# Performance work log

Hardware: AMD Instinct MI355X
Metric: run time of the kernel (lower is better)

## Reference

```python
import jax, jax.numpy as jnp
import numpy as np

B, N, C, H, DFF = 4, 1024, 768, 12, 3072
D = C // H
EPS = 1e-5


def _layernorm(x, w, b, axes):
    mu = jnp.mean(x, axis=axes, keepdims=True)
    var = jnp.mean(jnp.square(x - mu), axis=axes, keepdims=True)
    return (x - mu) * jax.lax.rsqrt(var + EPS) * w + b


def setup_inputs() -> dict:
    key = jax.random.key(0)
    ks = jax.random.split(key, 8)
    s = lambda fan_in: 1.0 / np.sqrt(fan_in)
    return {
        'x': jax.random.normal(ks[0], (B, N, C), jnp.float32),
        'ln0_w': jnp.ones((C,), jnp.float32),
        'ln0_b': jnp.zeros((C,), jnp.float32),
        'qkv_w': jax.random.normal(ks[1], (3 * C, C), jnp.float32) * s(C),
        'qkv_b': jax.random.normal(ks[2], (3 * C,), jnp.float32) * 0.01,
        'proj_w': jax.random.normal(ks[3], (C, C), jnp.float32) * s(C),
        'proj_b': jax.random.normal(ks[4], (C,), jnp.float32) * 0.01,
        'attn_norm_w': jnp.ones((H, N, N), jnp.float32),
        'attn_norm_b': jnp.zeros((H, N, N), jnp.float32),
        'ln1_w': jnp.ones((C,), jnp.float32),
        'ln1_b': jnp.zeros((C,), jnp.float32),
        'fc1_w': jax.random.normal(ks[5], (DFF, C), jnp.float32) * s(C),
        'fc1_b': jax.random.normal(ks[6], (DFF,), jnp.float32) * 0.01,
        'fc2_w': jax.random.normal(ks[7], (C, DFF), jnp.float32) * s(DFF),
        'fc2_b': jnp.zeros((C,), jnp.float32),
    }


def reference(x, ln0_w, ln0_b, qkv_w, qkv_b, proj_w, proj_b,
              attn_norm_w, attn_norm_b, ln1_w, ln1_b,
              fc1_w, fc1_b, fc2_w, fc2_b):
    # pre-norm
    h = _layernorm(x, ln0_w, ln0_b, axes=-1)
    # qkv projection -> (3, B, H, N, D)
    qkv = (h @ qkv_w.T + qkv_b).reshape(B, N, 3, H, D).transpose(2, 0, 3, 1, 4)
    q, k, v = qkv[0], qkv[1], qkv[2]
    # grassmanian_point: project each head vector onto the unit sphere
    q = q / jnp.linalg.norm(q, axis=-1, keepdims=True)
    k = k / jnp.linalg.norm(k, axis=-1, keepdims=True)
    # sum_d (q_{id} k_{jd})^2  ==  (q^2) @ (k^2)^T   -- avoids (B,H,D,N,N) tensor
    attn = jnp.einsum('bhid,bhjd->bhij', jnp.square(q), jnp.square(k))
    # LayerNorm over (H, N, N) jointly per batch element
    attn = _layernorm(attn, attn_norm_w, attn_norm_b, axes=(1, 2, 3))
    out = jnp.einsum('bhij,bhjd->bhid', attn, v)
    out = out.transpose(0, 2, 1, 3).reshape(B, N, C)
    out = out @ proj_w.T + proj_b
    # residual + post-norm + FFN (dropout/drop_path are identity in eval)
    src = x + out
    src = _layernorm(src, ln1_w, ln1_b, axes=-1)
    ff = jax.nn.gelu(src @ fc1_w.T + fc1_b, approximate=False) @ fc2_w.T + fc2_b
    src = src + ff
    return src, attn
```

## Files before the change

### kernel.cpp

```cpp
#include <hip/hip_runtime.h>

typedef __bf16 bf16;
typedef __bf16 bf16x4 __attribute__((ext_vector_type(4)));
typedef __bf16 bf16x8 __attribute__((ext_vector_type(8)));
typedef float f32x4 __attribute__((ext_vector_type(4)));

#define DEVI __device__ __forceinline__

typedef const __attribute__((address_space(1))) void* gas1;
typedef __attribute__((address_space(3))) void* las3;

DEVI int xcd_chunk(int bid, int nwg)
{
  const int q = nwg >> 3, r = nwg & 7;
  const int xcd = bid & 7, rank = bid >> 3;
  return (xcd < r) ? xcd * (q + 1) + rank
                   : r * (q + 1) + (xcd - r) * q + rank;
}

DEVI void stage_tile(const bf16* g, int ld, char* lds, int bytes, int tid)
{
  const int wv = tid >> 6, lane = tid & 63;
  const char* gb = (const char*)g;
  const long rowb = (long)ld * 2;
  for (int off = wv * 1024; off < bytes; off += 4096) {
    const int o  = off + lane * 16;
    const int s  = o ^ (((o >> 7) & 7) << 4);
    const int r  = s >> 7;
    const int cb = s & 127;
    __builtin_amdgcn_global_load_lds((gas1)(gb + (long)r * rowb + cb),
                                     (las3)(lds + off), 16, 0, 0);
  }
}

template<int N> DEVI void waitvm()
{
  if constexpr (N == 8)      asm volatile("s_waitcnt vmcnt(8)" ::: "memory");
  else if constexpr (N == 6) asm volatile("s_waitcnt vmcnt(6)" ::: "memory");
  else if constexpr (N == 4) asm volatile("s_waitcnt vmcnt(4)" ::: "memory");
  else if constexpr (N == 2) asm volatile("s_waitcnt vmcnt(2)" ::: "memory");
  else                       asm volatile("s_waitcnt vmcnt(0)" ::: "memory");
}

DEVI void wave_lds_fence()
{
  asm volatile("s_waitcnt lgkmcnt(0)" ::: "memory");
  __builtin_amdgcn_sched_barrier(0);
}

struct EpiProj {
  const float* bias; const float* x; float* src;
  DEVI void operator()(int z, int row, int col, float v) const {
    const long i = (long)row * 768 + col;
    src[i] = v + bias[col] + x[i];
  }
};

struct EpiGelu {
  const float* bias; bf16* g;
  DEVI void operator()(int z, int row, int col, float v) const {
    const float t = v + bias[col];
    const float r = 0.5f * t * (1.0f + erff(t * 0.70710678118654752f));
    g[(long)row * 3072 + col] = (bf16)r;
  }
};

struct EpiOut {
  const float* bias; const float* lnf; float* outp;
  DEVI void operator()(int z, int row, int col, float v) const {
    const long i = (long)row * 768 + col;
    outp[i] = v + bias[col] + lnf[i];
  }
};

template<int BM, int BN, int WC, int FM, int FN, int WPE, class Epi>
__global__ __launch_bounds__(256, WPE) void gemm_k(
    const bf16* __restrict__ A, long abatch,
    const bf16* __restrict__ B, long bbatch,
    int lda, int ldb, int K, Epi epi)
{
  constexpr int BK = 64;
  constexpr int AB = BM * BK * 2, BB = BN * BK * 2;
  constexpr int BUFB = AB + BB;
  constexpr int LPS = BUFB / 4096;
  __shared__ char smem[2 * BUFB];

  const int tid = threadIdx.x, lane = tid & 63, wv = tid >> 6;
  const int wr = wv / WC, wc = wv % WC;
  const int NT = gridDim.x;
  const int nwg = NT * gridDim.y;
  const int wid = xcd_chunk(blockIdx.y * NT + blockIdx.x, nwg);
  const int mt = wid / NT, nt = wid % NT;
  const int z = blockIdx.z;
  const long abase = (long)z * abatch + (long)mt * BM * lda;
  const long bbase = (long)z * bbatch + (long)nt * BN * ldb;
  const int l15 = lane & 15;
  const int sw = (lane & 7) << 4;

  auto stage_all = [&](int buf, int kt) {
    char* base = smem + buf * BUFB;
    stage_tile(A + abase + kt, lda, base, AB, tid);
    stage_tile(B + bbase + kt, ldb, base + AB, BB, tid);
  };

  f32x4 acc[FM][FN];
#pragma unroll
  for (int m = 0; m < FM; ++m)
#pragma unroll
    for (int n = 0; n < FN; ++n) acc[m][n] = f32x4{0.f, 0.f, 0.f, 0.f};

  const int arow = wr * FM * 16, bcol = wc * FN * 16;
  const int T = K / BK;

  stage_all(0, 0);
  int cur = 0;
  for (int t = 0; t < T; ++t) {
    if (t + 1 < T) { stage_all(cur ^ 1, (t + 1) * BK); waitvm<LPS>(); }
    else           { waitvm<0>(); }
    __builtin_amdgcn_s_barrier();
    asm volatile("" ::: "memory");

    const char* As = smem + cur * BUFB;
    const char* Bs = As + AB;
#pragma unroll
    for (int ks = 0; ks < 2; ++ks) {
      const int ko = (ks * 64 + (lane >> 4) * 16) ^ sw;
      bf16x8 av[FM], bv[FN];
#pragma unroll
      for (int m = 0; m < FM; ++m)
        av[m] = *(const bf16x8*)(As + (arow + m * 16 + l15) * 128 + ko);
#pragma unroll
      for (int n = 0; n < FN; ++n)
        bv[n] = *(const bf16x8*)(Bs + (bcol + n * 16 + l15) * 128 + ko);
#pragma unroll
      for (int m = 0; m < FM; ++m)
#pragma unroll
        for (int n = 0; n < FN; ++n)
          acc[m][n] = __builtin_amdgcn_mfma_f32_16x16x32_bf16(av[m], bv[n], acc[m][n], 0, 0, 0);
    }
    asm volatile("s_waitcnt lgkmcnt(0)" ::: "memory");
    __builtin_amdgcn_s_barrier();
    asm volatile("" ::: "memory");
    cur ^= 1;
  }

#pragma unroll
  for (int m = 0; m < FM; ++m)
#pragma unroll
    for (int n = 0; n < FN; ++n)
#pragma unroll
      for (int r = 0; r < 4; ++r) {
        const int grow = mt * BM + arow + m * 16 + (lane >> 4) * 4 + r;
        const int gcol = nt * BN + bcol + n * 16 + l15;
        epi(z, grow, gcol, acc[m][n][r]);
      }
}

__global__ __launch_bounds__(256, 3) void gemm_qkv(
    const bf16* __restrict__ A, const bf16* __restrict__ B,
    const float* __restrict__ bias, bf16* __restrict__ q2h,
    bf16* __restrict__ k2h, bf16* __restrict__ vth)
{
  constexpr int BM = 128, BN = 64, BK = 64;
  constexpr int AB = BM * BK * 2, BB = BN * BK * 2;
  constexpr int BUFB = AB + BB;
  constexpr int LPS = BUFB / 4096;
  __shared__ char smem[2 * BUFB];
  __shared__ float rowsum[2][BM];

  const int tid = threadIdx.x, lane = tid & 63, wv = tid >> 6;
  const int wr = wv >> 1, wc = wv & 1;
  const int NT = 36;
  const int wid = xcd_chunk(blockIdx.y * NT + blockIdx.x, NT * 32);
  const int mt = wid / NT, nt = wid % NT;
  const int sec = nt / 12, h = nt - sec * 12;
  const long abase = (long)mt * BM * 768;
  const long bbase = (long)nt * BN * 768;
  const int l15 = lane & 15, lhi = lane >> 4;
  const int sw = (lane & 7) << 4;

  auto stage_all = [&](int buf, int kt) {
    char* base = smem + buf * BUFB;
    stage_tile(A + abase + kt, 768, base, AB, tid);
    stage_tile(B + bbase + kt, 768, base + AB, BB, tid);
  };

  f32x4 acc[4][2];
#pragma unroll
  for (int m = 0; m < 4; ++m)
#pragma unroll
    for (int n = 0; n < 2; ++n) acc[m][n] = f32x4{0.f, 0.f, 0.f, 0.f};

  const int arow = wr * 64, bcol = wc * 32;

  stage_all(0, 0);
  int cur = 0;
  for (int t = 0; t < 12; ++t) {
    if (t + 1 < 12) { stage_all(cur ^ 1, (t + 1) * BK); waitvm<LPS>(); }
    else            { waitvm<0>(); }
    __builtin_amdgcn_s_barrier();
    asm volatile("" ::: "memory");

    const char* As = smem + cur * BUFB;
    const char* Bs = As + AB;
#pragma unroll
    for (int ks = 0; ks < 2; ++ks) {
      const int ko = (ks * 64 + lhi * 16) ^ sw;
      bf16x8 av[4], bv[2];
#pragma unroll
      for (int m = 0; m < 4; ++m)
        av[m] = *(const bf16x8*)(As + (arow + m * 16 + l15) * 128 + ko);
#pragma unroll
      for (int n = 0; n < 2; ++n)
        bv[n] = *(const bf16x8*)(Bs + (bcol + n * 16 + l15) * 128 + ko);
#pragma unroll
      for (int m = 0; m < 4; ++m)
#pragma unroll
        for (int n = 0; n < 2; ++n)
          acc[m][n] = __builtin_amdgcn_mfma_f32_16x16x32_bf16(av[m], bv[n], acc[m][n], 0, 0, 0);
    }
    asm volatile("s_waitcnt lgkmcnt(0)" ::: "memory");
    __builtin_amdgcn_s_barrier();
    asm volatile("" ::: "memory");
    cur ^= 1;
  }

  float val[4][2][4];
#pragma unroll
  for (int m = 0; m < 4; ++m)
#pragma unroll
    for (int n = 0; n < 2; ++n)
#pragma unroll
      for (int r = 0; r < 4; ++r)
        val[m][n][r] = acc[m][n][r] + bias[nt * 64 + bcol + n * 16 + l15];

  if (sec < 2) {
#pragma unroll
    for (int m = 0; m < 4; ++m)
#pragma unroll
      for (int r = 0; r < 4; ++r) {
        float p = val[m][0][r] * val[m][0][r] + val[m][1][r] * val[m][1][r];
        p += __shfl_xor(p, 1);
        p += __shfl_xor(p, 2);
        p += __shfl_xor(p, 4);
        p += __shfl_xor(p, 8);
        if (l15 == 0) rowsum[wc][arow + m * 16 + lhi * 4 + r] = p;
      }
    __syncthreads();
    bf16* dst = (sec == 0) ? q2h : k2h;
#pragma unroll
    for (int m = 0; m < 4; ++m)
#pragma unroll
      for (int r = 0; r < 4; ++r) {
        const int row = arow + m * 16 + lhi * 4 + r;
        const float inv = 1.0f / (rowsum[0][row] + rowsum[1][row]);
        const int grow = mt * BM + row;
        const int b = grow >> 10, nn = grow & 1023;
        const long base = (((long)(b * 12 + h)) * 1024 + nn) * 64;
#pragma unroll
        for (int n = 0; n < 2; ++n) {
          const float v = val[m][n][r];
          dst[base + bcol + n * 16 + l15] = (bf16)(v * v * inv);
        }
      }
  } else {
    bf16* T = (bf16*)smem;
#pragma unroll
    for (int m = 0; m < 4; ++m)
#pragma unroll
      for (int n = 0; n < 2; ++n)
#pragma unroll
        for (int r = 0; r < 4; ++r) {
          const int row = arow + m * 16 + lhi * 4 + r;
          const int col = bcol + n * 16 + l15;
          T[col * 144 + row] = (bf16)val[m][n][r];
        }
    __syncthreads();
    const int bq = mt >> 3, nn0 = (mt & 7) * 128;
    const long basez = ((long)(bq * 12 + h) * 64) * 1024;
#pragma unroll
    for (int it = 0; it < 4; ++it) {
      const int flat = it * 2048 + tid * 8;
      const int d = flat >> 7, c = flat & 127;
      const bf16x8 o = *(const bf16x8*)&T[d * 144 + c];
      *(bf16x8*)&vth[basez + (long)d * 1024 + nn0 + c] = o;
    }
  }
}

__global__ __launch_bounds__(256, 3) void attn_fused(
    const bf16* __restrict__ q2h, const bf16* __restrict__ k2h,
    const bf16* __restrict__ vth, const float* __restrict__ stats,
    const float* __restrict__ wn, const float* __restrict__ bn,
    float* __restrict__ attn_out, bf16* __restrict__ oh)
{
  __shared__ char smem[49152];
  char* Qs  = smem;
  char* Ks0 = smem + 8192;
  char* Ks1 = smem + 16384;
  char* Vs0 = smem + 24576;
  char* Vs1 = smem + 32768;
  char* Pall = smem + 40960;

  const int tid = threadIdx.x, lane = tid & 63, wv = tid >> 6;
  const int wid = xcd_chunk(blockIdx.x, 768);
  const int b = wid & 3;
  const int mt = (wid >> 2) & 15;
  const int h = wid >> 6;
  const int zq = b * 12 + h;
  const float mu = stats[2 * b], rs = stats[2 * b + 1];
  const int l15 = lane & 15, lhi = lane >> 4;
  const int sw = (lane & 7) << 4;
  char* Ps = Pall + wv * 2048;

  const long zoff = (long)zq * 65536;

  auto load_wb = [&](int nt, f32x4* wreg, f32x4* breg) {
#pragma unroll
    for (int rr = 0; rr < 4; ++rr) {
      const long grow = (long)mt * 64 + wv * 16 + rr * 4 + lhi;
      const long gcol = (long)nt * 64 + l15 * 4;
      wreg[rr] = *(const f32x4*)&wn[((long)h * 1024 + grow) * 1024 + gcol];
      breg[rr] = *(const f32x4*)&bn[((long)h * 1024 + grow) * 1024 + gcol];
    }
  };

  f32x4 wcur[4], bcur[4];
  load_wb(0, wcur, bcur);
  stage_tile(q2h + zoff + (long)mt * 4096, 64, Qs, 8192, tid);
  stage_tile(k2h + zoff, 64, Ks0, 8192, tid);
  stage_tile(vth + zoff, 1024, Vs0, 8192, tid);
  __syncthreads();

  f32x4 oacc[4];
#pragma unroll
  for (int n = 0; n < 4; ++n) oacc[n] = f32x4{0.f, 0.f, 0.f, 0.f};

  for (int nt = 0; nt < 16; ++nt) {
    const int cur = nt & 1;
    char* Kc = cur ? Ks1 : Ks0;
    char* Vc = cur ? Vs1 : Vs0;
    char* Kn = cur ? Ks0 : Ks1;
    char* Vn = cur ? Vs0 : Vs1;

    f32x4 wnx[4], bnx[4];
    if (nt + 1 < 16) {
      load_wb(nt + 1, wnx, bnx);
      stage_tile(k2h + zoff + (long)(nt + 1) * 4096, 64, Kn, 8192, tid);
      stage_tile(vth + zoff + (nt + 1) * 64, 1024, Vn, 8192, tid);
    }

    f32x4 acc[4];
#pragma unroll
    for (int n = 0; n < 4; ++n) acc[n] = f32x4{0.f, 0.f, 0.f, 0.f};
    __builtin_amdgcn_s_setprio(1);
#pragma unroll
    for (int ks = 0; ks < 2; ++ks) {
      const int ko = (ks * 64 + lhi * 16) ^ sw;
      const bf16x8 av = *(const bf16x8*)(Qs + (wv * 16 + l15) * 128 + ko);
#pragma unroll
      for (int n = 0; n < 4; ++n) {
        const bf16x8 bv = *(const bf16x8*)(Kc + (n * 16 + l15) * 128 + ko);
        acc[n] = __builtin_amdgcn_mfma_f32_16x16x32_bf16(av, bv, acc[n], 0, 0, 0);
      }
    }
    __builtin_amdgcn_s_setprio(0);
#pragma unroll
    for (int n = 0; n < 4; ++n)
#pragma unroll
      for (int r = 0; r < 4; ++r) {
        const int row = lhi * 4 + r;
        const int cb = (n * 32 + l15 * 2) ^ ((row & 7) << 4);
        *(bf16*)(Ps + row * 128 + cb) = (bf16)((acc[n][r] - mu) * rs);
      }
    wave_lds_fence();

#pragma unroll
    for (int rr = 0; rr < 4; ++rr) {
      const int row = rr * 4 + lhi;
      const int cb = (l15 * 8) ^ ((row & 7) << 4);
      const bf16x4 s4 = *(const bf16x4*)(Ps + row * 128 + cb);
      const long grow = (long)mt * 64 + wv * 16 + row;
      const long gcol = (long)nt * 64 + l15 * 4;
      f32x4 r4;
      bf16x4 h4;
#pragma unroll
      for (int e = 0; e < 4; ++e) {
        const float r = (float)s4[e] * wcur[rr][e] + bcur[rr][e];
        r4[e] = r;
        h4[e] = (bf16)r;
      }
      *(f32x4*)&attn_out[((long)zq * 1024 + grow) * 1024 + gcol] = r4;
      *(bf16x4*)(Ps + row * 128 + cb) = h4;
    }
    wave_lds_fence();

    __builtin_amdgcn_s_setprio(1);
#pragma unroll
    for (int ks = 0; ks < 2; ++ks) {
      const int ko = (ks * 64 + lhi * 16) ^ sw;
      const bf16x8 av = *(const bf16x8*)(Ps + l15 * 128 + ko);
#pragma unroll
      for (int n = 0; n < 4; ++n) {
        const bf16x8 bv = *(const bf16x8*)(Vc + (n * 16 + l15) * 128 + ko);
        oacc[n] = __builtin_amdgcn_mfma_f32_16x16x32_bf16(av, bv, oacc[n], 0, 0, 0);
      }
    }
    __builtin_amdgcn_s_setprio(0);
    waitvm<4>();
    __builtin_amdgcn_s_barrier();
    asm volatile("" ::: "memory");

    if (nt + 1 < 16) {
#pragma unroll
      for (int rr = 0; rr < 4; ++rr) { wcur[rr] = wnx[rr]; bcur[rr] = bnx[rr]; }
    }
  }

#pragma unroll
  for (int n = 0; n < 4; ++n)
#pragma unroll
    for (int r = 0; r < 4; ++r) {
      const int row = mt * 64 + wv * 16 + lhi * 4 + r;
      const int col = n * 16 + l15;
      oh[((long)(b * 1024 + row)) * 768 + h * 64 + col] = (bf16)oacc[n][r];
    }
}

__global__ void cast_all(const float* __restrict__ qkvw, const float* __restrict__ projw,
                         const float* __restrict__ fc1w, const float* __restrict__ fc2w,
                         bf16* __restrict__ dq, bf16* __restrict__ dp,
                         bf16* __restrict__ d1, bf16* __restrict__ d2)
{
  const int i = blockIdx.x * 256 + threadIdx.x;
  const float* s; bf16* d; int off;
  if (i < 442368)       { s = qkvw; d = dq; off = i; }
  else if (i < 589824)  { s = projw; d = dp; off = i - 442368; }
  else if (i < 1179648) { s = fc1w; d = d1; off = i - 589824; }
  else                  { s = fc2w; d = d2; off = i - 1179648; }
  const f32x4 v = *(const f32x4*)&s[(long)off * 4];
  bf16x4 o;
#pragma unroll
  for (int j = 0; j < 4; ++j) o[j] = (bf16)v[j];
  *(bf16x4*)&d[(long)off * 4] = o;
}

__global__ __launch_bounds__(256) void ln_row(
    const float* __restrict__ in, const float* __restrict__ w,
    const float* __restrict__ b, bf16* __restrict__ outh,
    float* __restrict__ outf)
{
  __shared__ float red[256];
  const int row = blockIdx.x, tid = threadIdx.x;
  const float* p = in + (long)row * 768;
  const float v0 = p[tid], v1 = p[tid + 256], v2 = p[tid + 512];
  red[tid] = v0 + v1 + v2;
  __syncthreads();
  for (int st = 128; st > 0; st >>= 1) { if (tid < st) red[tid] += red[tid + st]; __syncthreads(); }
  const float mu = red[0] * (1.0f / 768.0f);
  __syncthreads();
  const float d0 = v0 - mu, d1 = v1 - mu, d2 = v2 - mu;
  red[tid] = d0 * d0 + d1 * d1 + d2 * d2;
  __syncthreads();
  for (int st = 128; st > 0; st >>= 1) { if (tid < st) red[tid] += red[tid + st]; __syncthreads(); }
  const float rs = rsqrtf(red[0] * (1.0f / 768.0f) + 1e-5f);
  const float dv[3] = {d0, d1, d2};
#pragma unroll
  for (int k = 0; k < 3; ++k) {
    const int c = tid + k * 256;
    const float h = dv[k] * rs * w[c] + b[c];
    outh[(long)row * 768 + c] = (bf16)h;
    if (outf) outf[(long)row * 768 + c] = h;
  }
}

__global__ __launch_bounds__(256) void stats_accum(
    const bf16* __restrict__ q2h, const bf16* __restrict__ k2h,
    float* __restrict__ Gq, float* __restrict__ Gk,
    float* __restrict__ Sq, float* __restrict__ Sk)
{
  __shared__ float rowbuf[8][128];
  const int tid = threadIdx.x;
  const int z = blockIdx.y;
  const long base = ((long)z * 1024 + (long)blockIdx.x * 128) * 64;
  const int tx = tid & 15, ty = tid >> 4;
  float gq[4][4] = {}, gk[4][4] = {};
  float sq = 0.f, sk = 0.f;
  for (int r0 = 0; r0 < 128; r0 += 8) {
    __syncthreads();
    {
      const int idx = tid * 4;
      const int rr = idx >> 7, cc = idx & 127;
      const long a = base + (long)(r0 + rr) * 64 + (cc & 63);
      const bf16x4 v4 = (cc < 64) ? *(const bf16x4*)&q2h[a]
                                  : *(const bf16x4*)&k2h[a];
#pragma unroll
      for (int j = 0; j < 4; ++j) rowbuf[rr][cc + j] = (float)v4[j];
    }
    __syncthreads();
#pragma unroll
    for (int r = 0; r < 8; ++r) {
      float qa[4], qe[4], ka[4], ke[4];
#pragma unroll
      for (int i = 0; i < 4; ++i) {
        qa[i] = rowbuf[r][ty * 4 + i]; qe[i] = rowbuf[r][tx * 4 + i];
        ka[i] = rowbuf[r][64 + ty * 4 + i]; ke[i] = rowbuf[r][64 + tx * 4 + i];
      }
#pragma unroll
      for (int i = 0; i < 4; ++i)
#pragma unroll
        for (int j = 0; j < 4; ++j) {
          gq[i][j] += qa[i] * qe[j];
          gk[i][j] += ka[i] * ke[j];
        }
    }
    if (tid < 128) {
      float s = 0.f;
#pragma unroll
      for (int r = 0; r < 8; ++r) s += rowbuf[r][tid];
      if (tid < 64) sq += s; else sk += s;
    }
  }
#pragma unroll
  for (int i = 0; i < 4; ++i)
#pragma unroll
    for (int j = 0; j < 4; ++j) {
      atomicAdd(&Gq[(long)z * 4096 + (ty * 4 + i) * 64 + tx * 4 + j], gq[i][j]);
      atomicAdd(&Gk[(long)z * 4096 + (ty * 4 + i) * 64 + tx * 4 + j], gk[i][j]);
    }
  if (tid < 64) atomicAdd(&Sq[z * 64 + tid], sq);
  else if (tid < 128) atomicAdd(&Sk[z * 64 + tid - 64], sk);
}

__global__ __launch_bounds__(256) void stats_final(
    const float* __restrict__ Gq, const float* __restrict__ Gk,
    const float* __restrict__ Sq, const float* __restrict__ Sk,
    float* __restrict__ stats)
{
  __shared__ double red[256];
  const int b = blockIdx.x, tid = threadIdx.x;
  double s2 = 0.0, s1 = 0.0;
  for (int h = 0; h < 12; ++h) {
    const float* gq = Gq + ((long)(b * 12 + h)) * 4096;
    const float* gk = Gk + ((long)(b * 12 + h)) * 4096;
    for (int i = tid; i < 4096; i += 256) s2 += (double)gq[i] * (double)gk[i];
    const float* sqp = Sq + (b * 12 + h) * 64;
    const float* skp = Sk + (b * 12 + h) * 64;
    for (int i = tid; i < 64; i += 256) s1 += (double)sqp[i] * (double)skp[i];
  }
  red[tid] = s2; __syncthreads();
  for (int st = 128; st > 0; st >>= 1) { if (tid < st) red[tid] += red[tid + st]; __syncthreads(); }
  const double S2 = red[0]; __syncthreads();
  red[tid] = s1; __syncthreads();
  for (int st = 128; st > 0; st >>= 1) { if (tid < st) red[tid] += red[tid + st]; __syncthreads(); }
  if (tid == 0) {
    const double S1 = red[0];
    const double cnt = 12.0 * 1024.0 * 1024.0;
    const double mean = S1 / cnt;
    const double var = S2 / cnt - mean * mean;
    stats[2 * b] = (float)mean;
    stats[2 * b + 1] = (float)(1.0 / sqrt(var + 1e-5));
  }
}

extern "C" void kernel_launch(void* const* d_in, const int* in_sizes, int n_in,
                              void* d_out, int out_size, void* d_ws, size_t ws_size,
                              hipStream_t stream)
{
  const float* x      = (const float*)d_in[0];
  const float* ln0_w  = (const float*)d_in[1];
  const float* ln0_b  = (const float*)d_in[2];
  const float* qkv_w  = (const float*)d_in[3];
  const float* qkv_b  = (const float*)d_in[4];
  const float* proj_w = (const float*)d_in[5];
  const float* proj_b = (const float*)d_in[6];
  const float* attn_w = (const float*)d_in[7];
  const float* attn_b = (const float*)d_in[8];
  const float* ln1_w  = (const float*)d_in[9];
  const float* ln1_b  = (const float*)d_in[10];
  const float* fc1_w  = (const float*)d_in[11];
  const float* fc1_b  = (const float*)d_in[12];
  const float* fc2_w  = (const float*)d_in[13];
  const float* fc2_b  = (const float*)d_in[14];

  float* out_src  = (float*)d_out;
  float* out_attn = out_src + 4L * 1024 * 768;

  char* p = (char*)d_ws;
  auto take = [&](long bytes) -> char* {
    char* r = p;
    p += (bytes + 255) & ~255L;
    return r;
  };
  bf16* qkvw_h = (bf16*)take(3538944);
  bf16* projw_h = (bf16*)take(1179648);
  bf16* fc1w_h = (bf16*)take(4718592);
  bf16* fc2w_h = (bf16*)take(4718592);
  char* regB = take(12582912);
  bf16* hh = (bf16*)regB;
  float* src = (float*)regB;
  char* regC = take(37748736);
  bf16* gact = (bf16*)regC;
  float* ln1f = (float*)(regC + 25165824);
  bf16* q2h = (bf16*)take(6291456);
  bf16* k2h = (bf16*)take(6291456);
  bf16* vth = (bf16*)take(6291456);
  bf16* oh  = (bf16*)take(6291456);
  bf16* h1v = (bf16*)take(6291456);
  float* Gq = (float*)take(786432);
  float* Gk = (float*)take(786432);
  float* Sq = (float*)take(12288);
  float* Sk = (float*)take(12288);
  float* stats = (float*)take(256);

  const dim3 blk(256);

  (void)hipMemsetAsync((void*)Gq, 0, 786432 * 2 + 12288 * 2 + 256, stream);

  cast_all<<<dim3(1769472 / 256), blk, 0, stream>>>(
      qkv_w, proj_w, fc1_w, fc2_w, qkvw_h, projw_h, fc1w_h, fc2w_h);

  ln_row<<<dim3(4096), blk, 0, stream>>>(x, ln0_w, ln0_b, hh, nullptr);

  gemm_qkv<<<dim3(36, 32), blk, 0, stream>>>(
      hh, qkvw_h, qkv_b, q2h, k2h, vth);

  stats_accum<<<dim3(8, 48), blk, 0, stream>>>(q2h, k2h, Gq, Gk, Sq, Sk);
  stats_final<<<dim3(4), blk, 0, stream>>>(Gq, Gk, Sq, Sk, stats);

  attn_fused<<<dim3(768), blk, 0, stream>>>(
      q2h, k2h, vth, stats, attn_w, attn_b, out_attn, oh);

  gemm_k<128, 64, 2, 4, 2, 3, EpiProj><<<dim3(12, 32, 1), blk, 0, stream>>>(
      oh, 0, projw_h, 0, 768, 768, 768, EpiProj{proj_b, x, src});

  ln_row<<<dim3(4096), blk, 0, stream>>>(src, ln1_w, ln1_b, h1v, ln1f);

  gemm_k<128, 64, 2, 4, 2, 3, EpiGelu><<<dim3(48, 32, 1), blk, 0, stream>>>(
      h1v, 0, fc1w_h, 0, 768, 768, 768, EpiGelu{fc1_b, gact});

  gemm_k<128, 64, 2, 4, 2, 3, EpiOut><<<dim3(12, 32, 1), blk, 0, stream>>>(
      gact, 0, fc2w_h, 0, 3072, 3072, 3072, EpiOut{fc2_b, ln1f, out_src});
}
```

Baseline: 364.9 us.

## Fuse Gram statistics into QKV GEMM epilogue and merge weight cast with LayerNorm

The q²/k² Gram matrices and column sums used for the attention LayerNorm statistics are now computed inside the QKV GEMM epilogue. Each tile is staged into swizzled LDS, multiplied with MFMA and accumulated with atomics, which removes the separate stats_accum kernel and its re-read of q2h/k2h. The weight cast and the first LayerNorm are also merged into one prep launch to cut a kernel launch. In exchange the GEMM epilogue does extra LDS traffic, MFMA work and many more global atomics per tile.

```diff
diff --git a/kernel.cpp b/kernel.cpp
--- a/kernel.cpp
+++ b/kernel.cpp
@@ -159,7 +159,9 @@
 __global__ __launch_bounds__(256, 3) void gemm_qkv(
     const bf16* __restrict__ A, const bf16* __restrict__ B,
     const float* __restrict__ bias, bf16* __restrict__ q2h,
-    bf16* __restrict__ k2h, bf16* __restrict__ vth)
+    bf16* __restrict__ k2h, bf16* __restrict__ vth,
+    float* __restrict__ Gq, float* __restrict__ Gk,
+    float* __restrict__ Sq, float* __restrict__ Sk)
 {
   constexpr int BM = 128, BN = 64, BK = 64;
   constexpr int AB = BM * BK * 2, BB = BN * BK * 2;
@@ -247,7 +249,15 @@
         if (l15 == 0) rowsum[wc][arow + m * 16 + lhi * 4 + r] = p;
       }
     __syncthreads();
+
     bf16* dst = (sec == 0) ? q2h : k2h;
+    float* G  = (sec == 0) ? Gq  : Gk;
+    float* S  = (sec == 0) ? Sq  : Sk;
+    const int bq = mt >> 3;
+    const int z = bq * 12 + h;
+    char* T0 = smem;
+    char* T1 = smem + 8192;
+    float colsum[2] = {0.f, 0.f};
 #pragma unroll
     for (int m = 0; m < 4; ++m)
 #pragma unroll
@@ -255,14 +265,47 @@
         const int row = arow + m * 16 + lhi * 4 + r;
         const float inv = 1.0f / (rowsum[0][row] + rowsum[1][row]);
         const int grow = mt * BM + row;
-        const int b = grow >> 10, nn = grow & 1023;
-        const long base = (((long)(b * 12 + h)) * 1024 + nn) * 64;
+        const int nn = grow & 1023;
+        const long base = (((long)z) * 1024 + nn) * 64;
+        char* Tt = (row & 64) ? T1 : T0;
+        const int np = row & 63;
 #pragma unroll
         for (int n = 0; n < 2; ++n) {
           const float v = val[m][n][r];
-          dst[base + bcol + n * 16 + l15] = (bf16)(v * v * inv);
+          const int d = bcol + n * 16 + l15;
+          const bf16 q2b = (bf16)(v * v * inv);
+          dst[base + d] = q2b;
+          *(bf16*)(Tt + d * 128 + ((np * 2) ^ ((d & 7) << 4))) = q2b;
+          colsum[n] += (float)q2b;
         }
       }
+#pragma unroll
+    for (int n = 0; n < 2; ++n) {
+      float s = colsum[n];
+      s += __shfl_xor(s, 16);
+      s += __shfl_xor(s, 32);
+      if (lane < 16) atomicAdd(&S[z * 64 + bcol + n * 16 + l15], s);
+    }
+    __syncthreads();
+
+#pragma unroll
+    for (int gi = 0; gi < 4; ++gi) {
+      const int g = wv * 4 + gi;
+      const int dr = g >> 2, ec = g & 3;
+      f32x4 ga = f32x4{0.f, 0.f, 0.f, 0.f};
+#pragma unroll
+      for (int ks = 0; ks < 4; ++ks) {
+        const char* Tt = (ks & 2) ? T1 : T0;
+        const int ko = ((ks & 1) * 64 + lhi * 16) ^ sw;
+        const bf16x8 av = *(const bf16x8*)(Tt + (dr * 16 + l15) * 128 + ko);
+        const bf16x8 bv = *(const bf16x8*)(Tt + (ec * 16 + l15) * 128 + ko);
+        ga = __builtin_amdgcn_mfma_f32_16x16x32_bf16(av, bv, ga, 0, 0, 0);
+      }
+#pragma unroll
+      for (int r = 0; r < 4; ++r)
+        atomicAdd(&G[(long)z * 4096 + (dr * 16 + lhi * 4 + r) * 64 + ec * 16 + l15],
+                  ga[r]);
+    }
   } else {
     bf16* T = (bf16*)smem;
 #pragma unroll
@@ -427,22 +470,49 @@
     }
 }
 
-__global__ void cast_all(const float* __restrict__ qkvw, const float* __restrict__ projw,
-                         const float* __restrict__ fc1w, const float* __restrict__ fc2w,
-                         bf16* __restrict__ dq, bf16* __restrict__ dp,
-                         bf16* __restrict__ d1, bf16* __restrict__ d2)
-{
-  const int i = blockIdx.x * 256 + threadIdx.x;
-  const float* s; bf16* d; int off;
-  if (i < 442368)       { s = qkvw; d = dq; off = i; }
-  else if (i < 589824)  { s = projw; d = dp; off = i - 442368; }
-  else if (i < 1179648) { s = fc1w; d = d1; off = i - 589824; }
-  else                  { s = fc2w; d = d2; off = i - 1179648; }
-  const f32x4 v = *(const f32x4*)&s[(long)off * 4];
-  bf16x4 o;
-#pragma unroll
-  for (int j = 0; j < 4; ++j) o[j] = (bf16)v[j];
-  *(bf16x4*)&d[(long)off * 4] = o;
+__global__ __launch_bounds__(256) void prep(
+    const float* __restrict__ qkvw, const float* __restrict__ projw,
+    const float* __restrict__ fc1w, const float* __restrict__ fc2w,
+    bf16* __restrict__ dq, bf16* __restrict__ dp,
+    bf16* __restrict__ d1, bf16* __restrict__ d2,
+    const float* __restrict__ x, const float* __restrict__ w,
+    const float* __restrict__ bb, bf16* __restrict__ outh)
+{
+  __shared__ float red[256];
+  const int bid = blockIdx.x, tid = threadIdx.x;
+  if (bid < 6912) {
+    const int i = bid * 256 + tid;
+    const float* s; bf16* d; int off;
+    if (i < 442368)       { s = qkvw; d = dq; off = i; }
+    else if (i < 589824)  { s = projw; d = dp; off = i - 442368; }
+    else if (i < 1179648) { s = fc1w; d = d1; off = i - 589824; }
+    else                  { s = fc2w; d = d2; off = i - 1179648; }
+    const f32x4 v = *(const f32x4*)&s[(long)off * 4];
+    bf16x4 o;
+#pragma unroll
+    for (int j = 0; j < 4; ++j) o[j] = (bf16)v[j];
+    *(bf16x4*)&d[(long)off * 4] = o;
+  } else {
+    const int row = bid - 6912;
+    const float* p = x + (long)row * 768;
+    const float v0 = p[tid], v1 = p[tid + 256], v2 = p[tid + 512];
+    red[tid] = v0 + v1 + v2;
+    __syncthreads();
+    for (int st = 128; st > 0; st >>= 1) { if (tid < st) red[tid] += red[tid + st]; __syncthreads(); }
+    const float mu = red[0] * (1.0f / 768.0f);
+    __syncthreads();
+    const float d0 = v0 - mu, d1v = v1 - mu, d2v = v2 - mu;
+    red[tid] = d0 * d0 + d1v * d1v + d2v * d2v;
+    __syncthreads();
+    for (int st = 128; st > 0; st >>= 1) { if (tid < st) red[tid] += red[tid + st]; __syncthreads(); }
+    const float rs = rsqrtf(red[0] * (1.0f / 768.0f) + 1e-5f);
+    const float dv[3] = {d0, d1v, d2v};
+#pragma unroll
+    for (int k = 0; k < 3; ++k) {
+      const int c = tid + k * 256;
+      outh[(long)row * 768 + c] = (bf16)(dv[k] * rs * w[c] + bb[c]);
+    }
+  }
 }
 
 __global__ __launch_bounds__(256) void ln_row(
@@ -472,64 +542,6 @@
     outh[(long)row * 768 + c] = (bf16)h;
     if (outf) outf[(long)row * 768 + c] = h;
   }
-}
-
-__global__ __launch_bounds__(256) void stats_accum(
-    const bf16* __restrict__ q2h, const bf16* __restrict__ k2h,
-    float* __restrict__ Gq, float* __restrict__ Gk,
-    float* __restrict__ Sq, float* __restrict__ Sk)
-{
-  __shared__ float rowbuf[8][128];
-  const int tid = threadIdx.x;
-  const int z = blockIdx.y;
-  const long base = ((long)z * 1024 + (long)blockIdx.x * 128) * 64;
-  const int tx = tid & 15, ty = tid >> 4;
-  float gq[4][4] = {}, gk[4][4] = {};
-  float sq = 0.f, sk = 0.f;
-  for (int r0 = 0; r0 < 128; r0 += 8) {
-    __syncthreads();
-    {
-      const int idx = tid * 4;
-      const int rr = idx >> 7, cc = idx & 127;
-      const long a = base + (long)(r0 + rr) * 64 + (cc & 63);
-      const bf16x4 v4 = (cc < 64) ? *(const bf16x4*)&q2h[a]
-                                  : *(const bf16x4*)&k2h[a];
-#pragma unroll
-      for (int j = 0; j < 4; ++j) rowbuf[rr][cc + j] = (float)v4[j];
-    }
-    __syncthreads();
-#pragma unroll
-    for (int r = 0; r < 8; ++r) {
-      float qa[4], qe[4], ka[4], ke[4];
-#pragma unroll
-      for (int i = 0; i < 4; ++i) {
-        qa[i] = rowbuf[r][ty * 4 + i]; qe[i] = rowbuf[r][tx * 4 + i];
-        ka[i] = rowbuf[r][64 + ty * 4 + i]; ke[i] = rowbuf[r][64 + tx * 4 + i];
-      }
-#pragma unroll
-      for (int i = 0; i < 4; ++i)
-#pragma unroll
-        for (int j = 0; j < 4; ++j) {
-          gq[i][j] += qa[i] * qe[j];
-          gk[i][j] += ka[i] * ke[j];
-        }
-    }
-    if (tid < 128) {
-      float s = 0.f;
-#pragma unroll
-      for (int r = 0; r < 8; ++r) s += rowbuf[r][tid];
-      if (tid < 64) sq += s; else sk += s;
-    }
-  }
-#pragma unroll
-  for (int i = 0; i < 4; ++i)
-#pragma unroll
-    for (int j = 0; j < 4; ++j) {
-      atomicAdd(&Gq[(long)z * 4096 + (ty * 4 + i) * 64 + tx * 4 + j], gq[i][j]);
-      atomicAdd(&Gk[(long)z * 4096 + (ty * 4 + i) * 64 + tx * 4 + j], gk[i][j]);
-    }
-  if (tid < 64) atomicAdd(&Sq[z * 64 + tid], sq);
-  else if (tid < 128) atomicAdd(&Sk[z * 64 + tid - 64], sk);
 }
 
 __global__ __launch_bounds__(256) void stats_final(
@@ -617,15 +629,13 @@
 
   (void)hipMemsetAsync((void*)Gq, 0, 786432 * 2 + 12288 * 2 + 256, stream);
 
-  cast_all<<<dim3(1769472 / 256), blk, 0, stream>>>(
-      qkv_w, proj_w, fc1_w, fc2_w, qkvw_h, projw_h, fc1w_h, fc2w_h);
-
-  ln_row<<<dim3(4096), blk, 0, stream>>>(x, ln0_w, ln0_b, hh, nullptr);
+  prep<<<dim3(11008), blk, 0, stream>>>(
+      qkv_w, proj_w, fc1_w, fc2_w, qkvw_h, projw_h, fc1w_h, fc2w_h,
+      x, ln0_w, ln0_b, hh);
 
   gemm_qkv<<<dim3(36, 32), blk, 0, stream>>>(
-      hh, qkvw_h, qkv_b, q2h, k2h, vth);
-
-  stats_accum<<<dim3(8, 48), blk, 0, stream>>>(q2h, k2h, Gq, Gk, Sq, Sk);
+      hh, qkvw_h, qkv_b, q2h, k2h, vth, Gq, Gk, Sq, Sk);
+
   stats_final<<<dim3(4), blk, 0, stream>>>(Gq, Gk, Sq, Sk, stats);
 
   attn_fused<<<dim3(768), blk, 0, stream>>>(
```

Result: faster. 316.3 us, median of 2 (-13.3%).
